# Kernel tuning notes

Hardware: AMD Instinct MI355X
Metric: run time of the kernel (lower is better)

Reference implementation:

```python
import jax, jax.numpy as jnp
import numpy as np

N = 4096
DIM = 128      # dim_in
HID = 256      # mlp hidden_dim
K_IN = 8       # k for linear_k

def _knn_edges(dist, k):
    # dist: [n,n]; k nearest neighbors excluding self (matches heapq loop)
    n = dist.shape[0]
    d = jnp.where(jnp.eye(n, dtype=bool), jnp.inf, dist)
    nbr = jax.lax.top_k(-d, k)[1]                     # [n,k] indices of k smallest
    src = jnp.repeat(jnp.arange(n), k)                # res[0] = i
    dst = nbr.reshape(-1)                             # res[1] = neighbor
    return src, dst

def _gcn_conv(x, src, dst, W, b):
    # torch_geometric GCNConv: add self loops + symmetric normalization
    n = x.shape[0]
    loop = jnp.arange(n)
    s = jnp.concatenate([src, loop])
    t = jnp.concatenate([dst, loop])
    xw = x @ W
    deg = jax.ops.segment_sum(jnp.ones(s.shape[0], x.dtype), t, num_segments=n)
    dinv = jax.lax.rsqrt(deg)                         # deg >= 1 due to self loops
    norm = dinv[s] * dinv[t]
    out = jax.ops.segment_sum(norm[:, None] * xw[s], t, num_segments=n)
    return out + b

def _gcn(x, src, dst, Wg1, bg1, Wg2, bg2):
    h = jax.nn.relu(_gcn_conv(x, src, dst, Wg1, bg1))
    h = _gcn_conv(h, src, dst, Wg2, bg2)              # dropout is identity in eval
    return jax.nn.log_softmax(h, axis=1)

def _conv2d(x, w, b):
    y = jax.lax.conv_general_dilated(x, w, (1, 1), 'SAME',
        dimension_numbers=('NCHW', 'OIHW', 'NCHW'))
    return y + b.reshape(1, -1, 1, 1)

def setup_inputs():
    key = jax.random.key(0)
    ks = jax.random.split(key, 20)
    f32 = jnp.float32
    def w(k, shape):
        fan = shape[0]
        return (jax.random.uniform(k, shape, f32) * 2 - 1) * (1.0 / np.sqrt(fan))
    return {
        'data_x_1': jax.random.normal(ks[0], (1, N, 4), f32),
        'data_x_2': jax.random.normal(ks[1], (1, N, K_IN, 4), f32),
        'Wk': w(ks[2], (K_IN, 1)),        'bk': jnp.zeros((1,), f32),
        'Wg1': w(ks[3], (8, DIM // 2)),   'bg1': jnp.zeros((DIM // 2,), f32),
        'Wg2': w(ks[4], (DIM // 2, DIM)), 'bg2': jnp.zeros((DIM,), f32),
        'Wq': w(ks[5], (3 * DIM, DIM)),   'bq': jnp.zeros((DIM,), f32),
        'Wkey': w(ks[6], (3 * DIM, DIM)), 'bkey': jnp.zeros((DIM,), f32),
        'Woff': w(ks[7], (4, DIM)),       'boff': jnp.zeros((DIM,), f32),
        'pw': jnp.full((1,), 0.25, f32),
        'Wf1': w(ks[8], (DIM, HID)),      'bf1': jnp.zeros((HID,), f32),
        'Wf2': w(ks[9], (HID, HID)),      'bf2': jnp.zeros((HID,), f32),
        'Wf3': w(ks[10], (HID, 4)),       'bf3': jnp.zeros((4,), f32),
        'Wcy3': w(ks[11], (1, 1, 1, 3)),  'bcy3': jnp.zeros((1,), f32),
        'Wcx3': w(ks[12], (1, 1, 3, 1)),  'bcx3': jnp.zeros((1,), f32),
        'Wcy5': w(ks[13], (1, 1, 1, 5)),  'bcy5': jnp.zeros((1,), f32),
        'Wcx5': w(ks[14], (1, 1, 5, 1)),  'bcx5': jnp.zeros((1,), f32),
        'Wcy9': w(ks[15], (1, 1, 1, 9)),  'bcy9': jnp.zeros((1,), f32),
        'Wcx9': w(ks[16], (1, 1, 9, 1)),  'bcx9': jnp.zeros((1,), f32),
    }

def reference(data_x_1, data_x_2, Wk, bk, Wg1, bg1, Wg2, bg2, Wq, bq, Wkey, bkey,
              Woff, boff, pw, Wf1, bf1, Wf2, bf2, Wf3, bf3,
              Wcy3, bcy3, Wcx3, bcx3, Wcy5, bcy5, Wcx5, bcx5, Wcy9, bcy9, Wcx9, bcx9):
    # linear_k over k dimension: [1,n,k,4] -> transpose -> [1,n,4,k] -> [1,n,4]
    dx2 = jnp.swapaxes(data_x_2, 2, 3)
    dx2_out = (dx2 @ Wk + bk)[..., 0]
    data_x = jnp.concatenate([data_x_1, dx2_out], axis=2)   # [1,n,8]
    Ot = data_x[:, :, 4:]                                   # [1,n,4]

    pos = data_x[:, :, 0:2]
    diff = pos[:, :, None, :] - pos[:, None, :, :]          # [1,n,n,2]
    distances = jnp.linalg.norm(diff, axis=3)               # [1,n,n]
    maxd = jnp.max(distances, axis=2, keepdims=True)
    oushi_atte = 1.0 - distances / maxd                     # [1,n,n]

    x0 = data_x[0]
    dist0 = jax.lax.stop_gradient(distances[0])             # knn on detached dist
    embs = []
    for kk in (3, 5, 9):
        src, dst = _knn_edges(dist0, kk)
        embs.append(_gcn(x0, src, dst, Wg1, bg1, Wg2, bg2)[None])
    embedding = jnp.concatenate(embs, axis=2)               # [1,n,3*DIM]

    query = embedding @ Wq + bq                             # [1,n,DIM]
    key_t = embedding @ Wkey + bkey
    scores = jnp.einsum('bnd,bmd->bnm', query, key_t) / jnp.sqrt(jnp.float32(DIM))
    A = scores / jnp.max(scores, axis=2, keepdims=True)     # [1,n,n]

    A4 = A[None]                                            # [1,1,n,n]
    c3 = _conv2d(A4, Wcy3, bcy3) + _conv2d(A4, Wcx3, bcx3)
    c5 = _conv2d(A4, Wcy5, bcy5) + _conv2d(A4, Wcx5, bcx5)
    c9 = _conv2d(A4, Wcy9, bcy9) + _conv2d(A4, Wcx9, bcx9)

    A_cat = jnp.concatenate([A, oushi_atte, c3[0], c5[0], c9[0]], axis=2)  # [1,n,5n]
    A_cat = (A_cat - A_cat.min()) / (A_cat.max() - A_cat.min())

    Ot5 = jnp.tile(Ot, (1, 5, 1))                           # [1,5n,4]
    h = jnp.matmul(A_cat, Ot5)                              # [1,n,4]
    h = h @ Woff + boff                                     # [1,n,DIM]
    h = jnp.where(h > 0, h, pw * h)                         # PReLU (scalar weight)
    h = jax.nn.relu(h @ Wf1 + bf1)
    h = jax.nn.relu(h @ Wf2 + bf2)
    return h @ Wf3 + bf3                                    # [1,n,4]
```

## Files before the change

kernel.cpp:

```cpp
#include <hip/hip_runtime.h>
#include <math.h>

#define NN 4096

static __device__ __forceinline__ unsigned enc_f(float f){
    unsigned u = __float_as_uint(f);
    return (u & 0x80000000u) ? ~u : (u | 0x80000000u);
}
static __device__ __forceinline__ float dec_f(unsigned u){
    unsigned b = (u & 0x80000000u) ? (u & 0x7fffffffu) : ~u;
    return __uint_as_float(b);
}

__global__ void k_prep(const float* __restrict__ dx1, const float* __restrict__ dx2,
                       const float* __restrict__ Wk, const float* __restrict__ bk,
                       float* __restrict__ x0, float* __restrict__ colsum){
    int n = blockIdx.x*blockDim.x + threadIdx.x;
    if (n >= NN) return;
    float wk[8];
    #pragma unroll
    for (int j=0;j<8;j++) wk[j] = Wk[j];
    float bkv = bk[0];
    #pragma unroll
    for (int c=0;c<4;c++) x0[n*8+c] = dx1[n*4+c];
    #pragma unroll
    for (int c=0;c<4;c++){
        float acc = bkv;
        #pragma unroll
        for (int j=0;j<8;j++) acc += dx2[(n*8+j)*4+c]*wk[j];
        x0[n*8+4+c] = acc;
        atomicAdd(&colsum[c], acc);
    }
}

__global__ __launch_bounds__(256) void k_dist(const float* __restrict__ dx1,
        float* __restrict__ maxd, int* __restrict__ nbr,
        int* __restrict__ cnt3, int* __restrict__ cnt5, int* __restrict__ cnt9){
    __shared__ float2 ps[NN];
    int tid = threadIdx.x;
    for (int j=tid; j<NN; j+=256){
        float4 v = *(const float4*)&dx1[j*4];
        ps[j] = make_float2(v.x, v.y);
    }
    __syncthreads();
    int lane = tid & 63;
    int i = blockIdx.x*4 + (tid>>6);
    float2 pi = ps[i];
    unsigned long long best[9];
    #pragma unroll
    for (int q=0;q<9;q++) best[q] = ~0ULL;
    float lmax = 0.f;
    for (int t=0;t<64;t++){
        int j = (t<<6) | lane;
        float2 p = ps[j];
        float dx = pi.x - p.x, dy = pi.y - p.y;
        float d = sqrtf(dx*dx + dy*dy);
        lmax = fmaxf(lmax, d);
        unsigned long long cand = ((unsigned long long)__float_as_uint(d) << 32) | (unsigned)j;
        if (j != i && cand < best[8]){
            best[8] = cand;
            #pragma unroll
            for (int q=8; q>0; --q){
                if (best[q] < best[q-1]){ unsigned long long tm=best[q]; best[q]=best[q-1]; best[q-1]=tm; }
            }
        }
    }
    #pragma unroll
    for (int m=1;m<64;m<<=1) lmax = fmaxf(lmax, __shfl_xor(lmax, m, 64));
    if (lane==0) maxd[i] = lmax;
    for (int t=0;t<9;t++){
        unsigned long long w = best[0];
        #pragma unroll
        for (int m=1;m<64;m<<=1){
            unsigned long long o = __shfl_xor(w, m, 64);
            if (o < w) w = o;
        }
        if (best[0] == w){
            #pragma unroll
            for (int q=0;q<8;q++) best[q] = best[q+1];
            best[8] = ~0ULL;
        }
        if (lane==0){
            int j = (int)(w & 0xffffffffu);
            nbr[i*9+t] = j;
            atomicAdd(&cnt9[j], 1);
            if (t<5) atomicAdd(&cnt5[j], 1);
            if (t<3) atomicAdd(&cnt3[j], 1);
        }
    }
}

__global__ __launch_bounds__(256) void k_scan(const int* __restrict__ cnt3,
        const int* __restrict__ cnt5, const int* __restrict__ cnt9,
        int* __restrict__ offc, float* __restrict__ dinvc){
    __shared__ int part[256];
    int tid = threadIdx.x;
    for (int g=0; g<3; g++){
        const int* cp = g==0?cnt3:(g==1?cnt5:cnt9);
        int base = tid*16;
        int loc[16]; int s=0;
        #pragma unroll
        for (int q=0;q<16;q++){ loc[q]=s; s += cp[base+q]; }
        part[tid]=s; __syncthreads();
        for (int d=1; d<256; d<<=1){
            int v = (tid>=d) ? part[tid-d] : 0;
            __syncthreads();
            part[tid] += v;
            __syncthreads();
        }
        int pre = (tid==0) ? 0 : part[tid-1];
        #pragma unroll
        for (int q=0;q<16;q++){
            offc[g*NN + base + q]  = pre + loc[q];
            dinvc[g*NN + base + q] = rsqrtf((float)cp[base+q] + 1.f);
        }
        __syncthreads();
    }
}

__global__ void k_fill(const int* __restrict__ nbr, const int* __restrict__ offc,
        int* __restrict__ cur, int* __restrict__ rev){
    int i = blockIdx.x*256 + threadIdx.x;
    if (i >= NN) return;
    #pragma unroll
    for (int t=0;t<9;t++){
        int j = nbr[i*9+t];
        int gmin = t<3 ? 0 : (t<5 ? 1 : 2);
        for (int g=gmin; g<3; g++){
            int pos = atomicAdd(&cur[g*NN+j], 1);
            int rb = (g==0) ? 0 : (g==1 ? NN*3 : NN*8);
            rev[rb + offc[g*NN+j] + pos] = i;
        }
    }
}

__global__ void k_y1(const float* __restrict__ x0, const float* __restrict__ Wg1,
                     float* __restrict__ xw){
    int idx = blockIdx.x*256 + threadIdx.x;
    if (idx >= NN*64) return;
    int n = idx>>6, c = idx&63;
    float acc = 0.f;
    #pragma unroll
    for (int k=0;k<8;k++) acc += x0[n*8+k]*Wg1[k*64+c];
    xw[idx] = acc;
}

__global__ __launch_bounds__(256) void k_h1y2(const float* __restrict__ xw,
        const int* __restrict__ offc,
        const int* __restrict__ cnt3, const int* __restrict__ cnt5, const int* __restrict__ cnt9,
        const int* __restrict__ rev, const float* __restrict__ dinvc,
        const float* __restrict__ bg1, const float* __restrict__ Wg2,
        float* __restrict__ y2){
    __shared__ float h1s[12][64];
    int n0 = blockIdx.x*4, tid = threadIdx.x;
    for (int s=tid; s<768; s+=256){
        int p = s>>6, k = s&63, g = p>>2, n = n0+(p&3);
        const int* cp = g==0?cnt3:(g==1?cnt5:cnt9);
        int rb = (g==0) ? 0 : (g==1 ? NN*3 : NN*8);
        int cnt = cp[n];
        int o = rb + offc[g*NN+n];
        float dv = dinvc[g*NN+n];
        float srow = dv*xw[n*64+k];
        for (int e=0;e<cnt;e++){
            int i = rev[o+e];
            srow += dinvc[g*NN+i]*xw[i*64+k];
        }
        float v = dv*srow + bg1[k];
        h1s[p][k] = v>0.f ? v : 0.f;
    }
    __syncthreads();
    int c = tid & 127, ph = tid>>7;
    float a6[6] = {0,0,0,0,0,0};
    for (int k=0;k<64;k++){
        float w = Wg2[k*128+c];
        #pragma unroll
        for (int q=0;q<6;q++) a6[q] += h1s[q*2+ph][k]*w;
    }
    #pragma unroll
    for (int q=0;q<6;q++){
        int p = q*2+ph, g = p>>2, n = n0+(p&3);
        float dv = dinvc[g*NN+n];
        y2[(size_t)g*NN*128 + (size_t)n*128 + c] = dv*a6[q];
    }
}

__global__ __launch_bounds__(128) void k_fin(const float* __restrict__ y2,
        const int* __restrict__ offc,
        const int* __restrict__ cnt3, const int* __restrict__ cnt5, const int* __restrict__ cnt9,
        const int* __restrict__ rev, const float* __restrict__ dinvc,
        const float* __restrict__ bg2, float* __restrict__ emb){
    __shared__ float sm[2], ss[2];
    int b = blockIdx.x;
    int n = b & (NN-1), g = b >> 12;
    const int* cp = g==0?cnt3:(g==1?cnt5:cnt9);
    int rb = (g==0) ? 0 : (g==1 ? NN*3 : NN*8);
    int cnt = cp[n];
    int o = rb + offc[g*NN+n];
    float dv = dinvc[g*NN+n];
    int c = threadIdx.x;
    const float* yg = y2 + (size_t)g*NN*128;
    float s = yg[(size_t)n*128 + c];
    for (int e=0;e<cnt;e++){
        int i = rev[o+e];
        s += yg[(size_t)i*128 + c];
    }
    float v = dv*s + bg2[c];
    float m = v;
    #pragma unroll
    for (int st=1;st<64;st<<=1) m = fmaxf(m, __shfl_xor(m, st, 64));
    if ((c&63)==0) sm[c>>6] = m;
    __syncthreads();
    m = fmaxf(sm[0], sm[1]);
    float e = expf(v - m);
    float t = e;
    #pragma unroll
    for (int st=1;st<64;st<<=1) t += __shfl_xor(t, st, 64);
    if ((c&63)==0) ss[c>>6] = t;
    __syncthreads();
    t = ss[0]+ss[1];
    emb[n*384 + g*128 + c] = v - m - logf(t);
}

__global__ __launch_bounds__(256) void k_qk(const float* __restrict__ emb,
        const float* __restrict__ Wq, const float* __restrict__ bq,
        const float* __restrict__ Wkey, const float* __restrict__ bkey,
        float* __restrict__ q, float* __restrict__ kbuf){
    __shared__ float es[8][384];
    int n0 = blockIdx.x*8;
    int tid = threadIdx.x;
    for (int idx=tid; idx<8*384; idx+=256){
        int m = idx/384, k = idx%384;
        es[m][k] = emb[(n0+m)*384+k];
    }
    __syncthreads();
    int c = tid & 127;
    int sel = tid >> 7;
    const float* W = sel ? Wkey : Wq;
    float b = sel ? bkey[c] : bq[c];
    float acc[8];
    #pragma unroll
    for (int m=0;m<8;m++) acc[m]=b;
    for (int k=0;k<384;k++){
        float w = W[k*128+c];
        #pragma unroll
        for (int m=0;m<8;m++) acc[m] += es[m][k]*w;
    }
    float* out = sel ? kbuf : q;
    #pragma unroll
    for (int m=0;m<8;m++) out[(n0+m)*128+c] = acc[m];
}

__global__ __launch_bounds__(256) void k_scores(const float* __restrict__ q,
        const float* __restrict__ kb, float* __restrict__ scores,
        unsigned* __restrict__ rowmaxenc, unsigned* __restrict__ rowminenc){
    __shared__ float at[32][132];
    __shared__ float bt[32][132];
    int bx = blockIdx.x & 31;
    int by = blockIdx.x >> 5;
    int r0 = by*128, c0 = bx*128;
    int tid = threadIdx.x;
    int tx = tid & 15, ty = tid >> 4;
    float acc[8][8] = {};
    for (int k0 = 0; k0 < 128; k0 += 32){
        __syncthreads();
        #pragma unroll
        for (int l=0; l<4; l++){
            int idx = tid + l*256;
            int rowi = idx >> 3;
            int kq  = (idx & 7) * 4;
            float4 a = *(const float4*)&q [(size_t)(r0+rowi)*128 + k0 + kq];
            float4 b = *(const float4*)&kb[(size_t)(c0+rowi)*128 + k0 + kq];
            at[kq+0][rowi]=a.x; at[kq+1][rowi]=a.y; at[kq+2][rowi]=a.z; at[kq+3][rowi]=a.w;
            bt[kq+0][rowi]=b.x; bt[kq+1][rowi]=b.y; bt[kq+2][rowi]=b.z; bt[kq+3][rowi]=b.w;
        }
        __syncthreads();
        #pragma unroll
        for (int k=0;k<32;k++){
            float4 a0 = *(const float4*)&at[k][ty*4];
            float4 a1 = *(const float4*)&at[k][64+ty*4];
            float4 b0 = *(const float4*)&bt[k][tx*4];
            float4 b1 = *(const float4*)&bt[k][64+tx*4];
            float av[8] = {a0.x,a0.y,a0.z,a0.w,a1.x,a1.y,a1.z,a1.w};
            float bv[8] = {b0.x,b0.y,b0.z,b0.w,b1.x,b1.y,b1.z,b1.w};
            #pragma unroll
            for (int u=0;u<8;u++){
                #pragma unroll
                for (int v=0;v<8;v++) acc[u][v] += av[u]*bv[v];
            }
        }
    }
    #pragma unroll
    for (int u=0;u<8;u++){
        int rr = r0 + ((u<4)? ty*4+u : 64+ty*4+(u-4));
        float4 s0 = {acc[u][0],acc[u][1],acc[u][2],acc[u][3]};
        float4 s1 = {acc[u][4],acc[u][5],acc[u][6],acc[u][7]};
        *(float4*)&scores[(size_t)rr*NN + c0 + tx*4] = s0;
        *(float4*)&scores[(size_t)rr*NN + c0 + 64 + tx*4] = s1;
        float m = acc[u][0], mn = acc[u][0];
        #pragma unroll
        for (int v=1;v<8;v++){ m = fmaxf(m, acc[u][v]); mn = fminf(mn, acc[u][v]); }
        #pragma unroll
        for (int s=1;s<16;s<<=1){
            m  = fmaxf(m,  __shfl_xor(m,  s, 64));
            mn = fminf(mn, __shfl_xor(mn, s, 64));
        }
        if (tx==0){
            atomicMax(&rowmaxenc[rr], enc_f(m));
            atomicMin(&rowminenc[rr], enc_f(mn));
        }
    }
}

__global__ __launch_bounds__(256) void k_mcat(const float* __restrict__ scores,
        const unsigned* __restrict__ rowmaxenc, const float* __restrict__ maxd,
        const float* __restrict__ dx1, const float* __restrict__ x0,
        const float* __restrict__ Wcy3, const float* __restrict__ Wcx3,
        const float* __restrict__ Wcy5, const float* __restrict__ Wcx5,
        const float* __restrict__ Wcy9, const float* __restrict__ Wcx9,
        const float* __restrict__ bcy3, const float* __restrict__ bcx3,
        const float* __restrict__ bcy5, const float* __restrict__ bcx5,
        const float* __restrict__ bcy9, const float* __restrict__ bcx9,
        float* __restrict__ mnmx, float* __restrict__ hpart){
    __shared__ float As[72][96];
    __shared__ float invr_s[72];
    __shared__ float4 ots[64];
    __shared__ float2 pjv[64];
    __shared__ float2 piv[64];
    __shared__ float ims[64];
    __shared__ float smn[4], smx[4];
    int bx = blockIdx.x, by = blockIdx.y;
    int i0 = by*64, j0 = bx*64;
    int tid = threadIdx.x;

    float wy3[3],wx3[3],wy5[5],wx5[5],wy9[9],wx9[9];
    #pragma unroll
    for (int t=0;t<3;t++){ wy3[t]=Wcy3[t]; wx3[t]=Wcx3[t]; }
    #pragma unroll
    for (int t=0;t<5;t++){ wy5[t]=Wcy5[t]; wx5[t]=Wcx5[t]; }
    #pragma unroll
    for (int t=0;t<9;t++){ wy9[t]=Wcy9[t]; wx9[t]=Wcx9[t]; }
    float bc3 = bcy3[0]+bcx3[0];
    float bc5 = bcy5[0]+bcx5[0];
    float bc9 = bcy9[0]+bcx9[0];

    if (tid < 72){
        int gr = i0-4+tid;
        invr_s[tid] = ((unsigned)gr < NN) ? 1.f/dec_f(rowmaxenc[gr]) : 0.f;
    } else if (tid >= 96 && tid < 160){
        int c = tid-96, j = j0+c;
        float4 v = *(const float4*)&dx1[j*4];
        pjv[c] = make_float2(v.x, v.y);
        ots[c] = *(const float4*)&x0[j*8+4];
    } else if (tid >= 160 && tid < 224){
        int r = tid-160;
        float4 v = *(const float4*)&dx1[(i0+r)*4];
        piv[r] = make_float2(v.x, v.y);
        ims[r] = 1.f/maxd[i0+r];
    }
    __syncthreads();

    bool colEdge = (bx == 0) || (bx == 63);
    for (int s = tid; s < 72*20; s += 256){
        int row = s/20, c4 = s - row*20;
        int gr = i0 - 4 + row;
        int grc = gr < 0 ? 0 : (gr > NN-1 ? NN-1 : gr);
        int gcf = j0 - 8 + c4*4;
        float iv = invr_s[row];
        float4 v;
        if (!colEdge){
            v = *(const float4*)&scores[(size_t)grc*NN + gcf];
        } else {
            v = make_float4(0.f,0.f,0.f,0.f);
            const float* rp = &scores[(size_t)grc*NN];
            if ((unsigned)(gcf+0) < NN) v.x = rp[gcf+0];
            if ((unsigned)(gcf+1) < NN) v.y = rp[gcf+1];
            if ((unsigned)(gcf+2) < NN) v.z = rp[gcf+2];
            if ((unsigned)(gcf+3) < NN) v.w = rp[gcf+3];
        }
        int sc4 = c4 ^ ((row & 3) << 1);
        float* dst = &As[row][sc4*4];
        dst[0]=v.x*iv; dst[1]=v.y*iv; dst[2]=v.z*iv; dst[3]=v.w*iv;
    }
    __syncthreads();

    int rp = tid >> 3, cg = tid & 7;
    int r0l = rp*2;
    float mn = INFINITY, mx = -INFINITY;
    float pdx[2]={0,0}, pdy[2]={0,0}, pdz[2]={0,0}, pdw[2]={0,0};
    float2 prow0 = piv[r0l], prow1 = piv[r0l+1];
    float im0 = ims[r0l], im1 = ims[r0l+1];

    for (int h = 0; h < 2; ++h){
        int cbase = cg*8 + h*4;
        float colw[10][4];
        #pragma unroll
        for (int u=0; u<10; ++u){
            int row = r0l+u;
            int c4 = ((cbase+8)>>2) ^ ((row&3)<<1);
            float4 v = *(const float4*)&As[row][c4*4];
            colw[u][0]=v.x; colw[u][1]=v.y; colw[u][2]=v.z; colw[u][3]=v.w;
        }
        #pragma unroll
        for (int d=0; d<2; ++d){
            int row = r0l+4+d;
            float w[12];
            {
                int c4l = ((cbase+4)>>2) ^ ((row&3)<<1);
                int c4r = ((cbase+12)>>2) ^ ((row&3)<<1);
                float4 l = *(const float4*)&As[row][c4l*4];
                float4 rgt = *(const float4*)&As[row][c4r*4];
                w[0]=l.x; w[1]=l.y; w[2]=l.z; w[3]=l.w;
                #pragma unroll
                for (int k=0;k<4;++k) w[4+k] = colw[4+d][k];
                w[8]=rgt.x; w[9]=rgt.y; w[10]=rgt.z; w[11]=rgt.w;
            }
            float2 prow = d ? prow1 : prow0;
            float imv = d ? im1 : im0;
            #pragma unroll
            for (int c=0;c<4;++c){
                float cx9 = 0.f, cx5 = 0.f, cx3 = 0.f;
                #pragma unroll
                for (int u=0;u<9;++u) cx9 += colw[u+d][c]*wx9[u];
                #pragma unroll
                for (int u=0;u<5;++u) cx5 += colw[u+2+d][c]*wx5[u];
                #pragma unroll
                for (int u=0;u<3;++u) cx3 += colw[u+3+d][c]*wx3[u];
                float cy9 = bc9, cy5 = bc5, cy3 = bc3;
                #pragma unroll
                for (int u=0;u<9;++u) cy9 += w[c+u]*wy9[u];
                #pragma unroll
                for (int u=0;u<5;++u) cy5 += w[c+2+u]*wy5[u];
                #pragma unroll
                for (int u=0;u<3;++u) cy3 += w[c+3+u]*wy3[u];
                float c3v = cy3+cx3, c5v = cy5+cx5, c9v = cy9+cx9;
                mn = fminf(mn, fminf(fminf(c3v,c5v),c9v));
                mx = fmaxf(mx, fmaxf(fmaxf(c3v,c5v),c9v));
                float a = colw[4+d][c];
                float2 pj2 = pjv[cbase+c];
                float ddx = prow.x - pj2.x, ddy = prow.y - pj2.y;
                float ou = 1.f - sqrtf(ddx*ddx + ddy*ddy)*imv;
                float Mv = a + ou + c3v + c5v + c9v;
                float4 ot = ots[cbase+c];
                if (d==0){ pdx[0]+=Mv*ot.x; pdy[0]+=Mv*ot.y; pdz[0]+=Mv*ot.z; pdw[0]+=Mv*ot.w; }
                else     { pdx[1]+=Mv*ot.x; pdy[1]+=Mv*ot.y; pdz[1]+=Mv*ot.z; pdw[1]+=Mv*ot.w; }
            }
        }
    }
    #pragma unroll
    for (int m=1; m<8; m<<=1){
        #pragma unroll
        for (int d=0; d<2; ++d){
            pdx[d] += __shfl_xor(pdx[d], m, 64);
            pdy[d] += __shfl_xor(pdy[d], m, 64);
            pdz[d] += __shfl_xor(pdz[d], m, 64);
            pdw[d] += __shfl_xor(pdw[d], m, 64);
        }
    }
    if (cg == 0){
        #pragma unroll
        for (int d=0; d<2; ++d){
            float4 pd = {pdx[d], pdy[d], pdz[d], pdw[d]};
            *(float4*)&hpart[((size_t)(i0 + r0l + d)*64 + bx)*4] = pd;
        }
    }
    #pragma unroll
    for (int m=1; m<64; m<<=1){
        mn = fminf(mn, __shfl_xor(mn, m, 64));
        mx = fmaxf(mx, __shfl_xor(mx, m, 64));
    }
    int wid = tid >> 6;
    if ((tid & 63) == 0){ smn[wid] = mn; smx[wid] = mx; }
    __syncthreads();
    if (tid == 0){
        float a0 = fminf(fminf(smn[0],smn[1]), fminf(smn[2],smn[3]));
        float b0 = fmaxf(fmaxf(smx[0],smx[1]), fmaxf(smx[2],smx[3]));
        int bid = by*64 + bx;
        mnmx[bid] = a0;
        mnmx[4096 + bid] = b0;
    }
}

__global__ __launch_bounds__(256) void k_gmm(const float* __restrict__ mnmx,
        const unsigned* __restrict__ rowminenc, const unsigned* __restrict__ rowmaxenc,
        float* __restrict__ gmm){
    __shared__ float smn[256], smx[256];
    int tid = threadIdx.x;
    float mn = 0.f, mx = 1.f;
    for (int i=tid; i<4096; i+=256){
        mn = fminf(mn, mnmx[i]);
        mx = fmaxf(mx, mnmx[4096+i]);
        float rmx = dec_f(rowmaxenc[i]);
        float q = dec_f(rowminenc[i]) / rmx;
        mn = fminf(mn, fminf(1.f, q));
        mx = fmaxf(mx, fmaxf(1.f, q));
    }
    smn[tid]=mn; smx[tid]=mx; __syncthreads();
    for (int s=128;s>0;s>>=1){
        if (tid<s){ smn[tid]=fminf(smn[tid],smn[tid+s]); smx[tid]=fmaxf(smx[tid],smx[tid+s]); }
        __syncthreads();
    }
    if (tid==0){ gmm[0]=smn[0]; gmm[1]=smx[0]; }
}

__global__ __launch_bounds__(256) void k_hred(const float* __restrict__ hpart,
        const float* __restrict__ gmm, const float* __restrict__ colsum,
        float* __restrict__ hfin){
    int i = blockIdx.x*256 + threadIdx.x;
    if (i >= NN) return;
    float4 sum = {0,0,0,0};
    const float4* hp = (const float4*)hpart + (size_t)i*64;
    for (int xb=0; xb<64; xb++){
        float4 v = hp[xb];
        sum.x+=v.x; sum.y+=v.y; sum.z+=v.z; sum.w+=v.w;
    }
    float mnv = gmm[0], mxv = gmm[1];
    float s = 1.f/(mxv-mnv), o = -mnv*s;
    float4 cs = *(const float4*)colsum;
    float4 out;
    out.x = s*sum.x + 5.f*o*cs.x;
    out.y = s*sum.y + 5.f*o*cs.y;
    out.z = s*sum.z + 5.f*o*cs.z;
    out.w = s*sum.w + 5.f*o*cs.w;
    *(float4*)&hfin[i*4] = out;
}

__global__ __launch_bounds__(256) void k_mlp(const float* __restrict__ hfin,
        const float* __restrict__ Woff, const float* __restrict__ boff, const float* __restrict__ pw,
        const float* __restrict__ Wf1, const float* __restrict__ bf1,
        const float* __restrict__ Wf2, const float* __restrict__ bf2,
        const float* __restrict__ Wf3, const float* __restrict__ bf3,
        float* __restrict__ out){
    __shared__ float h1[8][128];
    __shared__ float h2[8][256];
    __shared__ float h3[8][256];
    __shared__ float4 red4[256];
    int n0 = blockIdx.x*8, tid = threadIdx.x;
    float p = pw[0];
    {
        int c = tid & 127, mb = (tid>>7)*4;
        #pragma unroll
        for (int mm=0; mm<4; mm++){
            int m = mb+mm;
            float v = boff[c];
            #pragma unroll
            for (int k=0;k<4;k++) v += hfin[(n0+m)*4+k]*Woff[k*128+c];
            h1[m][c] = v>0.f ? v : p*v;
        }
    }
    __syncthreads();
    {
        int c = tid;
        float acc[8];
        #pragma unroll
        for (int m=0;m<8;m++) acc[m] = bf1[c];
        for (int k=0;k<128;k++){
            float w = Wf1[k*256+c];
            #pragma unroll
            for (int m=0;m<8;m++) acc[m] += h1[m][k]*w;
        }
        #pragma unroll
        for (int m=0;m<8;m++) h2[m][c] = acc[m]>0.f?acc[m]:0.f;
    }
    __syncthreads();
    {
        int c = tid;
        float acc[8];
        #pragma unroll
        for (int m=0;m<8;m++) acc[m] = bf2[c];
        for (int k=0;k<256;k++){
            float w = Wf2[k*256+c];
            #pragma unroll
            for (int m=0;m<8;m++) acc[m] += h2[m][k]*w;
        }
        #pragma unroll
        for (int m=0;m<8;m++) h3[m][c] = acc[m]>0.f?acc[m]:0.f;
    }
    __syncthreads();
    float w3_0 = Wf3[tid*4+0], w3_1 = Wf3[tid*4+1], w3_2 = Wf3[tid*4+2], w3_3 = Wf3[tid*4+3];
    for (int m=0;m<8;m++){
        float hv = h3[m][tid];
        float4 r; r.x = hv*w3_0; r.y = hv*w3_1; r.z = hv*w3_2; r.w = hv*w3_3;
        red4[tid]=r; __syncthreads();
        for (int s=128;s>0;s>>=1){
            if(tid<s){
                red4[tid].x+=red4[tid+s].x; red4[tid].y+=red4[tid+s].y;
                red4[tid].z+=red4[tid+s].z; red4[tid].w+=red4[tid+s].w;
            }
            __syncthreads();
        }
        if (tid==0){
            float4 o;
            o.x = red4[0].x + bf3[0]; o.y = red4[0].y + bf3[1];
            o.z = red4[0].z + bf3[2]; o.w = red4[0].w + bf3[3];
            *(float4*)&out[(n0+m)*4] = o;
        }
        __syncthreads();
    }
}

extern "C" void kernel_launch(void* const* d_in, const int* in_sizes, int n_in,
                              void* d_out, int out_size, void* d_ws, size_t ws_size,
                              hipStream_t stream){
    const float* dx1  = (const float*)d_in[0];
    const float* dx2  = (const float*)d_in[1];
    const float* Wk   = (const float*)d_in[2];
    const float* bk   = (const float*)d_in[3];
    const float* Wg1  = (const float*)d_in[4];
    const float* bg1  = (const float*)d_in[5];
    const float* Wg2  = (const float*)d_in[6];
    const float* bg2  = (const float*)d_in[7];
    const float* Wq   = (const float*)d_in[8];
    const float* bq   = (const float*)d_in[9];
    const float* Wkey = (const float*)d_in[10];
    const float* bkey = (const float*)d_in[11];
    const float* Woff = (const float*)d_in[12];
    const float* boff = (const float*)d_in[13];
    const float* pw   = (const float*)d_in[14];
    const float* Wf1  = (const float*)d_in[15];
    const float* bf1  = (const float*)d_in[16];
    const float* Wf2  = (const float*)d_in[17];
    const float* bf2  = (const float*)d_in[18];
    const float* Wf3  = (const float*)d_in[19];
    const float* bf3  = (const float*)d_in[20];
    const float* Wcy3 = (const float*)d_in[21];
    const float* bcy3 = (const float*)d_in[22];
    const float* Wcx3 = (const float*)d_in[23];
    const float* bcx3 = (const float*)d_in[24];
    const float* Wcy5 = (const float*)d_in[25];
    const float* bcy5 = (const float*)d_in[26];
    const float* Wcx5 = (const float*)d_in[27];
    const float* bcx5 = (const float*)d_in[28];
    const float* Wcy9 = (const float*)d_in[29];
    const float* bcy9 = (const float*)d_in[30];
    const float* Wcx9 = (const float*)d_in[31];
    const float* bcx9 = (const float*)d_in[32];

    char* ws = (char*)d_ws;
    size_t off = 0;
    auto alloc = [&](size_t b)->void*{ void* p = ws + off; off += (b + 255) & ~(size_t)255; return p; };

    char* zbase = ws + off;
    float*    colsum    = (float*)   alloc(4*4);
    int*      cnt3      = (int*)     alloc((size_t)NN*4);
    int*      cnt5      = (int*)     alloc((size_t)NN*4);
    int*      cnt9      = (int*)     alloc((size_t)NN*4);
    int*      cur       = (int*)     alloc((size_t)3*NN*4);
    unsigned* rowmaxenc = (unsigned*)alloc((size_t)NN*4);
    size_t zbytes = (size_t)((ws + off) - zbase);
    unsigned* rowminenc = (unsigned*)alloc((size_t)NN*4);

    float* x0     = (float*)alloc((size_t)NN*8*4);
    float* maxd   = (float*)alloc((size_t)NN*4);
    int*   nbr    = (int*)  alloc((size_t)NN*9*4);
    int*   offc   = (int*)  alloc((size_t)3*NN*4);
    float* dinvc  = (float*)alloc((size_t)3*NN*4);
    int*   rev    = (int*)  alloc((size_t)NN*17*4);
    float* xw     = (float*)alloc((size_t)NN*64*4);
    float* y2     = (float*)alloc((size_t)3*NN*128*4);
    float* emb    = (float*)alloc((size_t)NN*384*4);
    float* qb     = (float*)alloc((size_t)NN*128*4);
    float* kb     = (float*)alloc((size_t)NN*128*4);
    float* scores = (float*)alloc((size_t)NN*NN*4);
    float* mnmx   = (float*)alloc((size_t)2*4096*4);
    float* hpart  = (float*)alloc((size_t)NN*64*4*4);
    float* gmm    = (float*)alloc(2*4);
    float* hfin   = (float*)alloc((size_t)NN*4*4);
    (void)ws_size; (void)in_sizes; (void)n_in; (void)out_size;

    hipMemsetAsync(zbase, 0, zbytes, stream);
    hipMemsetAsync(rowminenc, 0xFF, (size_t)NN*4, stream);

    k_prep<<<16,256,0,stream>>>(dx1,dx2,Wk,bk,x0,colsum);
    k_dist<<<NN/4,256,0,stream>>>(dx1,maxd,nbr,cnt3,cnt5,cnt9);
    k_scan<<<1,256,0,stream>>>(cnt3,cnt5,cnt9,offc,dinvc);
    k_fill<<<16,256,0,stream>>>(nbr,offc,cur,rev);

    k_y1  <<<NN*64/256,256,0,stream>>>(x0,Wg1,xw);
    k_h1y2<<<NN/4,256,0,stream>>>(xw,offc,cnt3,cnt5,cnt9,rev,dinvc,bg1,Wg2,y2);
    k_fin <<<NN*3,128,0,stream>>>(y2,offc,cnt3,cnt5,cnt9,rev,dinvc,bg2,emb);

    k_qk<<<NN/8,256,0,stream>>>(emb,Wq,bq,Wkey,bkey,qb,kb);
    k_scores<<<1024,256,0,stream>>>(qb,kb,scores,rowmaxenc,rowminenc);
    k_mcat<<<dim3(64,64),256,0,stream>>>(scores,rowmaxenc,maxd,dx1,x0,
        Wcy3,Wcx3,Wcy5,Wcx5,Wcy9,Wcx9,
        bcy3,bcx3,bcy5,bcx5,bcy9,bcx9, mnmx, hpart);
    k_gmm<<<1,256,0,stream>>>(mnmx,rowminenc,rowmaxenc,gmm);
    k_hred<<<NN/256,256,0,stream>>>(hpart,gmm,colsum,hfin);
    k_mlp<<<NN/8,256,0,stream>>>(hfin,Woff,boff,pw,Wf1,bf1,Wf2,bf2,Wf3,bf3,(float*)d_out);
}
```

Measured before the change: 335.0 us.

## Split conv/matmul fusion into streaming min/max pass and algebraic row-dot reduction

Reformulates the A_cat @ Ot5 product algebraically. Because the convolutions are linear, their contribution to h is computed as row dot-products of the scaled scores against Ot and against a precomputed vertically-convolved Ot (Ty), plus a horizontal 9-tap combination of those per-row results. The distance term is folded into the k_dist kernel as dOt. The convolution values themselves are still needed for the global min/max, so a new streaming kernel computes them per column with a rolling 9-row register window and wave-level LDS exchange, but no longer does the matmul. This removes the big hpart partial buffer and its reduction, at the cost of reading the scores matrix twice (k_cstream and k_rowdot) and changing floating-point summation order.

```diff
diff --git a/kernel.cpp b/kernel.cpp
--- a/kernel.cpp
+++ b/kernel.cpp
@@ -33,9 +33,37 @@
     }
 }
 
+__global__ void k_ty(const float* __restrict__ x0,
+        const float* __restrict__ Wcy3, const float* __restrict__ Wcy5, const float* __restrict__ Wcy9,
+        float* __restrict__ Ty){
+    int j = blockIdx.x*256 + threadIdx.x;
+    if (j >= NN) return;
+    float Cy[9];
+    #pragma unroll
+    for (int o=-4;o<=4;o++){
+        float c = Wcy9[o+4];
+        if (o>=-2 && o<=2) c += Wcy5[o+2];
+        if (o>=-1 && o<=1) c += Wcy3[o+1];
+        Cy[o+4] = c;
+    }
+    float4 acc = {0,0,0,0};
+    #pragma unroll
+    for (int o=-4;o<=4;o++){
+        int jj = j - o;
+        if ((unsigned)jj < NN){
+            float4 ot = *(const float4*)&x0[jj*8+4];
+            float c = Cy[o+4];
+            acc.x += c*ot.x; acc.y += c*ot.y; acc.z += c*ot.z; acc.w += c*ot.w;
+        }
+    }
+    *(float4*)&Ty[j*4] = acc;
+}
+
 __global__ __launch_bounds__(256) void k_dist(const float* __restrict__ dx1,
+        const float* __restrict__ x0,
         float* __restrict__ maxd, int* __restrict__ nbr,
-        int* __restrict__ cnt3, int* __restrict__ cnt5, int* __restrict__ cnt9){
+        int* __restrict__ cnt3, int* __restrict__ cnt5, int* __restrict__ cnt9,
+        float* __restrict__ dOt){
     __shared__ float2 ps[NN];
     int tid = threadIdx.x;
     for (int j=tid; j<NN; j+=256){
@@ -50,12 +78,15 @@
     #pragma unroll
     for (int q=0;q<9;q++) best[q] = ~0ULL;
     float lmax = 0.f;
+    float4 dacc = {0,0,0,0};
     for (int t=0;t<64;t++){
         int j = (t<<6) | lane;
         float2 p = ps[j];
         float dx = pi.x - p.x, dy = pi.y - p.y;
         float d = sqrtf(dx*dx + dy*dy);
         lmax = fmaxf(lmax, d);
+        float4 otj = *(const float4*)&x0[j*8+4];
+        dacc.x += d*otj.x; dacc.y += d*otj.y; dacc.z += d*otj.z; dacc.w += d*otj.w;
         unsigned long long cand = ((unsigned long long)__float_as_uint(d) << 32) | (unsigned)j;
         if (j != i && cand < best[8]){
             best[8] = cand;
@@ -66,8 +97,17 @@
         }
     }
     #pragma unroll
-    for (int m=1;m<64;m<<=1) lmax = fmaxf(lmax, __shfl_xor(lmax, m, 64));
-    if (lane==0) maxd[i] = lmax;
+    for (int m=1;m<64;m<<=1){
+        lmax = fmaxf(lmax, __shfl_xor(lmax, m, 64));
+        dacc.x += __shfl_xor(dacc.x, m, 64);
+        dacc.y += __shfl_xor(dacc.y, m, 64);
+        dacc.z += __shfl_xor(dacc.z, m, 64);
+        dacc.w += __shfl_xor(dacc.w, m, 64);
+    }
+    if (lane==0){
+        maxd[i] = lmax;
+        *(float4*)&dOt[i*4] = dacc;
+    }
     for (int t=0;t<9;t++){
         unsigned long long w = best[0];
         #pragma unroll
@@ -311,26 +351,31 @@
     }
 }
 
-__global__ __launch_bounds__(256) void k_mcat(const float* __restrict__ scores,
-        const unsigned* __restrict__ rowmaxenc, const float* __restrict__ maxd,
-        const float* __restrict__ dx1, const float* __restrict__ x0,
+__global__ void k_invr(const unsigned* __restrict__ rowmaxenc, const float* __restrict__ maxd,
+        float* __restrict__ invr, float* __restrict__ im){
+    int i = blockIdx.x*256 + threadIdx.x;
+    if (i >= NN) return;
+    invr[i] = 1.f/dec_f(rowmaxenc[i]);
+    im[i]   = 1.f/maxd[i];
+}
+
+__global__ __launch_bounds__(256) void k_cstream(const float* __restrict__ scores,
+        const float* __restrict__ invr,
         const float* __restrict__ Wcy3, const float* __restrict__ Wcx3,
         const float* __restrict__ Wcy5, const float* __restrict__ Wcx5,
         const float* __restrict__ Wcy9, const float* __restrict__ Wcx9,
         const float* __restrict__ bcy3, const float* __restrict__ bcx3,
         const float* __restrict__ bcy5, const float* __restrict__ bcx5,
         const float* __restrict__ bcy9, const float* __restrict__ bcx9,
-        float* __restrict__ mnmx, float* __restrict__ hpart){
-    __shared__ float As[72][96];
-    __shared__ float invr_s[72];
-    __shared__ float4 ots[64];
-    __shared__ float2 pjv[64];
-    __shared__ float2 piv[64];
-    __shared__ float ims[64];
+        float* __restrict__ mnmx){
+    __shared__ float rowbuf[4][80];
     __shared__ float smn[4], smx[4];
-    int bx = blockIdx.x, by = blockIdx.y;
-    int i0 = by*64, j0 = bx*64;
     int tid = threadIdx.x;
+    int w = tid >> 6, lane = tid & 63;
+    int jb = blockIdx.x*256 + w*64;
+    int j  = jb + lane;
+    int i0 = blockIdx.y*64;
+    volatile float* rb = rowbuf[w];
 
     float wy3[3],wx3[3],wy5[5],wx5[5],wy9[9],wx9[9];
     #pragma unroll
@@ -343,124 +388,60 @@
     float bc5 = bcy5[0]+bcx5[0];
     float bc9 = bcy9[0]+bcx9[0];
 
-    if (tid < 72){
-        int gr = i0-4+tid;
-        invr_s[tid] = ((unsigned)gr < NN) ? 1.f/dec_f(rowmaxenc[gr]) : 0.f;
-    } else if (tid >= 96 && tid < 160){
-        int c = tid-96, j = j0+c;
-        float4 v = *(const float4*)&dx1[j*4];
-        pjv[c] = make_float2(v.x, v.y);
-        ots[c] = *(const float4*)&x0[j*8+4];
-    } else if (tid >= 160 && tid < 224){
-        int r = tid-160;
-        float4 v = *(const float4*)&dx1[(i0+r)*4];
-        piv[r] = make_float2(v.x, v.y);
-        ims[r] = 1.f/maxd[i0+r];
-    }
-    __syncthreads();
-
-    bool colEdge = (bx == 0) || (bx == 63);
-    for (int s = tid; s < 72*20; s += 256){
-        int row = s/20, c4 = s - row*20;
-        int gr = i0 - 4 + row;
-        int grc = gr < 0 ? 0 : (gr > NN-1 ? NN-1 : gr);
-        int gcf = j0 - 8 + c4*4;
-        float iv = invr_s[row];
-        float4 v;
-        if (!colEdge){
-            v = *(const float4*)&scores[(size_t)grc*NN + gcf];
-        } else {
-            v = make_float4(0.f,0.f,0.f,0.f);
-            const float* rp = &scores[(size_t)grc*NN];
-            if ((unsigned)(gcf+0) < NN) v.x = rp[gcf+0];
-            if ((unsigned)(gcf+1) < NN) v.y = rp[gcf+1];
-            if ((unsigned)(gcf+2) < NN) v.z = rp[gcf+2];
-            if ((unsigned)(gcf+3) < NN) v.w = rp[gcf+3];
-        }
-        int sc4 = c4 ^ ((row & 3) << 1);
-        float* dst = &As[row][sc4*4];
-        dst[0]=v.x*iv; dst[1]=v.y*iv; dst[2]=v.z*iv; dst[3]=v.w*iv;
-    }
-    __syncthreads();
-
-    int rp = tid >> 3, cg = tid & 7;
-    int r0l = rp*2;
+    float win[9], cy3r[9], cy5r[9], cy9r[9];
     float mn = INFINITY, mx = -INFINITY;
-    float pdx[2]={0,0}, pdy[2]={0,0}, pdz[2]={0,0}, pdw[2]={0,0};
-    float2 prow0 = piv[r0l], prow1 = piv[r0l+1];
-    float im0 = ims[r0l], im1 = ims[r0l+1];
-
-    for (int h = 0; h < 2; ++h){
-        int cbase = cg*8 + h*4;
-        float colw[10][4];
-        #pragma unroll
-        for (int u=0; u<10; ++u){
-            int row = r0l+u;
-            int c4 = ((cbase+8)>>2) ^ ((row&3)<<1);
-            float4 v = *(const float4*)&As[row][c4*4];
-            colw[u][0]=v.x; colw[u][1]=v.y; colw[u][2]=v.z; colw[u][3]=v.w;
-        }
-        #pragma unroll
-        for (int d=0; d<2; ++d){
-            int row = r0l+4+d;
-            float w[12];
-            {
-                int c4l = ((cbase+4)>>2) ^ ((row&3)<<1);
-                int c4r = ((cbase+12)>>2) ^ ((row&3)<<1);
-                float4 l = *(const float4*)&As[row][c4l*4];
-                float4 rgt = *(const float4*)&As[row][c4r*4];
-                w[0]=l.x; w[1]=l.y; w[2]=l.z; w[3]=l.w;
-                #pragma unroll
-                for (int k=0;k<4;++k) w[4+k] = colw[4+d][k];
-                w[8]=rgt.x; w[9]=rgt.y; w[10]=rgt.z; w[11]=rgt.w;
+
+    bool haloL = (lane < 4);
+    bool haloR = (lane >= 60);
+    int jL = jb - 4 + lane;
+    int jR = jb + lane + 4;
+    bool vlL = haloL && (jL >= 0);
+    bool vlR = haloR && (jR < NN);
+
+    for (int tb = 0; tb < 8; ++tb){
+        #pragma unroll
+        for (int u = 0; u < 9; ++u){
+            int t  = tb*9 + u;
+            int ri = i0 - 4 + t;
+            bool rv = ((unsigned)ri < NN);
+            float iv = 0.f, v = 0.f, vL = 0.f, vR = 0.f;
+            if (rv){
+                iv = invr[ri];
+                const float* rp = scores + (size_t)ri*NN;
+                v = rp[j];
+                if (vlL) vL = rp[jL];
+                if (vlR) vR = rp[jR];
             }
-            float2 prow = d ? prow1 : prow0;
-            float imv = d ? im1 : im0;
+            float a = v*iv;
+            rb[lane+4] = a;
+            if (haloL) rb[lane]   = vL*iv;
+            if (haloR) rb[lane+8] = vR*iv;
+            __builtin_amdgcn_wave_barrier();
+            float tp[9];
             #pragma unroll
-            for (int c=0;c<4;++c){
-                float cx9 = 0.f, cx5 = 0.f, cx3 = 0.f;
-                #pragma unroll
-                for (int u=0;u<9;++u) cx9 += colw[u+d][c]*wx9[u];
-                #pragma unroll
-                for (int u=0;u<5;++u) cx5 += colw[u+2+d][c]*wx5[u];
-                #pragma unroll
-                for (int u=0;u<3;++u) cx3 += colw[u+3+d][c]*wx3[u];
-                float cy9 = bc9, cy5 = bc5, cy3 = bc3;
-                #pragma unroll
-                for (int u=0;u<9;++u) cy9 += w[c+u]*wy9[u];
-                #pragma unroll
-                for (int u=0;u<5;++u) cy5 += w[c+2+u]*wy5[u];
-                #pragma unroll
-                for (int u=0;u<3;++u) cy3 += w[c+3+u]*wy3[u];
-                float c3v = cy3+cx3, c5v = cy5+cx5, c9v = cy9+cx9;
-                mn = fminf(mn, fminf(fminf(c3v,c5v),c9v));
-                mx = fmaxf(mx, fmaxf(fmaxf(c3v,c5v),c9v));
-                float a = colw[4+d][c];
-                float2 pj2 = pjv[cbase+c];
-                float ddx = prow.x - pj2.x, ddy = prow.y - pj2.y;
-                float ou = 1.f - sqrtf(ddx*ddx + ddy*ddy)*imv;
-                float Mv = a + ou + c3v + c5v + c9v;
-                float4 ot = ots[cbase+c];
-                if (d==0){ pdx[0]+=Mv*ot.x; pdy[0]+=Mv*ot.y; pdz[0]+=Mv*ot.z; pdw[0]+=Mv*ot.w; }
-                else     { pdx[1]+=Mv*ot.x; pdy[1]+=Mv*ot.y; pdz[1]+=Mv*ot.z; pdw[1]+=Mv*ot.w; }
+            for (int k=0;k<9;k++) tp[k] = rb[lane+k];
+            __builtin_amdgcn_wave_barrier();
+            float cy9v = ((tp[0]*wy9[0] + tp[1]*wy9[1]) + (tp[2]*wy9[2] + tp[3]*wy9[3]))
+                       + ((tp[4]*wy9[4] + tp[5]*wy9[5]) + (tp[6]*wy9[6] + tp[7]*wy9[7]))
+                       + tp[8]*wy9[8];
+            float cy5v = ((tp[2]*wy5[0] + tp[3]*wy5[1]) + (tp[4]*wy5[2] + tp[5]*wy5[3]))
+                       + tp[6]*wy5[4];
+            float cy3v = (tp[3]*wy3[0] + tp[4]*wy3[1]) + tp[5]*wy3[2];
+            win[u]  = a;
+            cy3r[u] = cy3v; cy5r[u] = cy5v; cy9r[u] = cy9v;
+            if (t >= 8){
+                float cx9v = ((win[(u+1)%9]*wx9[0] + win[(u+2)%9]*wx9[1]) + (win[(u+3)%9]*wx9[2] + win[(u+4)%9]*wx9[3]))
+                           + ((win[(u+5)%9]*wx9[4] + win[(u+6)%9]*wx9[5]) + (win[(u+7)%9]*wx9[6] + win[(u+8)%9]*wx9[7]))
+                           + win[u]*wx9[8];
+                float cx5v = ((win[(u+3)%9]*wx5[0] + win[(u+4)%9]*wx5[1]) + (win[(u+5)%9]*wx5[2] + win[(u+6)%9]*wx5[3]))
+                           + win[(u+7)%9]*wx5[4];
+                float cx3v = (win[(u+4)%9]*wx3[0] + win[(u+5)%9]*wx3[1]) + win[(u+6)%9]*wx3[2];
+                float c9 = cy9r[(u+5)%9] + cx9v + bc9;
+                float c5 = cy5r[(u+5)%9] + cx5v + bc5;
+                float c3 = cy3r[(u+5)%9] + cx3v + bc3;
+                mn = fminf(mn, fminf(fminf(c3,c5),c9));
+                mx = fmaxf(mx, fmaxf(fmaxf(c3,c5),c9));
             }
-        }
-    }
-    #pragma unroll
-    for (int m=1; m<8; m<<=1){
-        #pragma unroll
-        for (int d=0; d<2; ++d){
-            pdx[d] += __shfl_xor(pdx[d], m, 64);
-            pdy[d] += __shfl_xor(pdy[d], m, 64);
-            pdz[d] += __shfl_xor(pdz[d], m, 64);
-            pdw[d] += __shfl_xor(pdw[d], m, 64);
-        }
-    }
-    if (cg == 0){
-        #pragma unroll
-        for (int d=0; d<2; ++d){
-            float4 pd = {pdx[d], pdy[d], pdz[d], pdw[d]};
-            *(float4*)&hpart[((size_t)(i0 + r0l + d)*64 + bx)*4] = pd;
         }
     }
     #pragma unroll
@@ -468,15 +449,59 @@
         mn = fminf(mn, __shfl_xor(mn, m, 64));
         mx = fmaxf(mx, __shfl_xor(mx, m, 64));
     }
-    int wid = tid >> 6;
-    if ((tid & 63) == 0){ smn[wid] = mn; smx[wid] = mx; }
+    if (lane == 0){ smn[w] = mn; smx[w] = mx; }
     __syncthreads();
     if (tid == 0){
         float a0 = fminf(fminf(smn[0],smn[1]), fminf(smn[2],smn[3]));
         float b0 = fmaxf(fmaxf(smx[0],smx[1]), fmaxf(smx[2],smx[3]));
-        int bid = by*64 + bx;
+        int bid = blockIdx.y*16 + blockIdx.x;
         mnmx[bid] = a0;
-        mnmx[4096 + bid] = b0;
+        mnmx[1024 + bid] = b0;
+    }
+}
+
+__global__ __launch_bounds__(256) void k_rowdot(const float* __restrict__ scores,
+        const float* __restrict__ x0, const float* __restrict__ Ty,
+        const float* __restrict__ invr, const float* __restrict__ im,
+        const float* __restrict__ dOt, const float* __restrict__ colsum,
+        const float* __restrict__ bcy3, const float* __restrict__ bcx3,
+        const float* __restrict__ bcy5, const float* __restrict__ bcx5,
+        const float* __restrict__ bcy9, const float* __restrict__ bcx9,
+        float* __restrict__ ASdot, float* __restrict__ Bv){
+    int tid = threadIdx.x;
+    int tc = tid & 31, tr = tid >> 5;
+    int i = blockIdx.x*8 + tr;
+    const float* srow = scores + (size_t)i*NN;
+    float4 ss = {0,0,0,0}, st = {0,0,0,0};
+    for (int c0 = tc; c0 < NN; c0 += 32){
+        float sv = srow[c0];
+        float4 ot = *(const float4*)&x0[c0*8+4];
+        float4 ty = *(const float4*)&Ty[c0*4];
+        ss.x += sv*ot.x; ss.y += sv*ot.y; ss.z += sv*ot.z; ss.w += sv*ot.w;
+        st.x += sv*ty.x; st.y += sv*ty.y; st.z += sv*ty.z; st.w += sv*ty.w;
+    }
+    #pragma unroll
+    for (int s=1; s<32; s<<=1){
+        ss.x += __shfl_xor(ss.x, s, 64); ss.y += __shfl_xor(ss.y, s, 64);
+        ss.z += __shfl_xor(ss.z, s, 64); ss.w += __shfl_xor(ss.w, s, 64);
+        st.x += __shfl_xor(st.x, s, 64); st.y += __shfl_xor(st.y, s, 64);
+        st.z += __shfl_xor(st.z, s, 64); st.w += __shfl_xor(st.w, s, 64);
+    }
+    if (tc == 0){
+        float iv = invr[i], imv = im[i];
+        float bcsum = bcy3[0]+bcx3[0]+bcy5[0]+bcx5[0]+bcy9[0]+bcx9[0];
+        float4 cs = *(const float4*)colsum;
+        float4 dv = *(const float4*)&dOt[i*4];
+        float4 as;
+        as.x = iv*ss.x; as.y = iv*ss.y; as.z = iv*ss.z; as.w = iv*ss.w;
+        float k = 1.f + bcsum;
+        float4 b;
+        b.x = cs.x*k - imv*dv.x + iv*st.x;
+        b.y = cs.y*k - imv*dv.y + iv*st.y;
+        b.z = cs.z*k - imv*dv.z + iv*st.z;
+        b.w = cs.w*k - imv*dv.w + iv*st.w;
+        *(float4*)&ASdot[i*4] = as;
+        *(float4*)&Bv[i*4]   = b;
     }
 }
 
@@ -486,14 +511,16 @@
     __shared__ float smn[256], smx[256];
     int tid = threadIdx.x;
     float mn = 0.f, mx = 1.f;
-    for (int i=tid; i<4096; i+=256){
-        mn = fminf(mn, mnmx[i]);
-        mx = fmaxf(mx, mnmx[4096+i]);
+    for (int i=tid; i<NN; i+=256){
         float rmx = dec_f(rowmaxenc[i]);
         float q = dec_f(rowminenc[i]) / rmx;
         mn = fminf(mn, fminf(1.f, q));
         mx = fmaxf(mx, fmaxf(1.f, q));
     }
+    for (int b=tid; b<1024; b+=256){
+        mn = fminf(mn, mnmx[b]);
+        mx = fmaxf(mx, mnmx[1024+b]);
+    }
     smn[tid]=mn; smx[tid]=mx; __syncthreads();
     for (int s=128;s>0;s>>=1){
         if (tid<s){ smn[tid]=fminf(smn[tid],smn[tid+s]); smx[tid]=fmaxf(smx[tid],smx[tid+s]); }
@@ -502,25 +529,40 @@
     if (tid==0){ gmm[0]=smn[0]; gmm[1]=smx[0]; }
 }
 
-__global__ __launch_bounds__(256) void k_hred(const float* __restrict__ hpart,
+__global__ void k_hfin(const float* __restrict__ ASdot, const float* __restrict__ Bv,
+        const float* __restrict__ Wcx3, const float* __restrict__ Wcx5, const float* __restrict__ Wcx9,
         const float* __restrict__ gmm, const float* __restrict__ colsum,
         float* __restrict__ hfin){
     int i = blockIdx.x*256 + threadIdx.x;
     if (i >= NN) return;
-    float4 sum = {0,0,0,0};
-    const float4* hp = (const float4*)hpart + (size_t)i*64;
-    for (int xb=0; xb<64; xb++){
-        float4 v = hp[xb];
-        sum.x+=v.x; sum.y+=v.y; sum.z+=v.z; sum.w+=v.w;
+    float Cx[9];
+    #pragma unroll
+    for (int o=-4;o<=4;o++){
+        float c = Wcx9[o+4];
+        if (o>=-2 && o<=2) c += Wcx5[o+2];
+        if (o>=-1 && o<=1) c += Wcx3[o+1];
+        Cx[o+4] = c;
+    }
+    float4 h = *(const float4*)&Bv[i*4];
+    float4 a0 = *(const float4*)&ASdot[i*4];
+    h.x += a0.x; h.y += a0.y; h.z += a0.z; h.w += a0.w;
+    #pragma unroll
+    for (int o=-4;o<=4;o++){
+        int r = i + o;
+        if ((unsigned)r < NN){
+            float4 av = *(const float4*)&ASdot[r*4];
+            float c = Cx[o+4];
+            h.x += c*av.x; h.y += c*av.y; h.z += c*av.z; h.w += c*av.w;
+        }
     }
     float mnv = gmm[0], mxv = gmm[1];
-    float s = 1.f/(mxv-mnv), o = -mnv*s;
+    float s = 1.f/(mxv-mnv), oa = -mnv*s;
     float4 cs = *(const float4*)colsum;
     float4 out;
-    out.x = s*sum.x + 5.f*o*cs.x;
-    out.y = s*sum.y + 5.f*o*cs.y;
-    out.z = s*sum.z + 5.f*o*cs.z;
-    out.w = s*sum.w + 5.f*o*cs.w;
+    out.x = s*h.x + 5.f*oa*cs.x;
+    out.y = s*h.y + 5.f*oa*cs.y;
+    out.z = s*h.z + 5.f*oa*cs.z;
+    out.w = s*h.w + 5.f*oa*cs.w;
     *(float4*)&hfin[i*4] = out;
 }
 
@@ -661,8 +703,13 @@
     float* qb     = (float*)alloc((size_t)NN*128*4);
     float* kb     = (float*)alloc((size_t)NN*128*4);
     float* scores = (float*)alloc((size_t)NN*NN*4);
-    float* mnmx   = (float*)alloc((size_t)2*4096*4);
-    float* hpart  = (float*)alloc((size_t)NN*64*4*4);
+    float* Tyb    = (float*)alloc((size_t)NN*4*4);
+    float* invr   = (float*)alloc((size_t)NN*4);
+    float* im     = (float*)alloc((size_t)NN*4);
+    float* dOt    = (float*)alloc((size_t)NN*4*4);
+    float* ASd    = (float*)alloc((size_t)NN*4*4);
+    float* Bv     = (float*)alloc((size_t)NN*4*4);
+    float* mnmx   = (float*)alloc((size_t)2*1024*4);
     float* gmm    = (float*)alloc(2*4);
     float* hfin   = (float*)alloc((size_t)NN*4*4);
     (void)ws_size; (void)in_sizes; (void)n_in; (void)out_size;
@@ -671,7 +718,8 @@
     hipMemsetAsync(rowminenc, 0xFF, (size_t)NN*4, stream);
 
     k_prep<<<16,256,0,stream>>>(dx1,dx2,Wk,bk,x0,colsum);
-    k_dist<<<NN/4,256,0,stream>>>(dx1,maxd,nbr,cnt3,cnt5,cnt9);
+    k_ty  <<<16,256,0,stream>>>(x0,Wcy3,Wcy5,Wcy9,Tyb);
+    k_dist<<<NN/4,256,0,stream>>>(dx1,x0,maxd,nbr,cnt3,cnt5,cnt9,dOt);
     k_scan<<<1,256,0,stream>>>(cnt3,cnt5,cnt9,offc,dinvc);
     k_fill<<<16,256,0,stream>>>(nbr,offc,cur,rev);
 
@@ -681,10 +729,14 @@
 
     k_qk<<<NN/8,256,0,stream>>>(emb,Wq,bq,Wkey,bkey,qb,kb);
     k_scores<<<1024,256,0,stream>>>(qb,kb,scores,rowmaxenc,rowminenc);
-    k_mcat<<<dim3(64,64),256,0,stream>>>(scores,rowmaxenc,maxd,dx1,x0,
+    k_invr<<<16,256,0,stream>>>(rowmaxenc,maxd,invr,im);
+
+    k_cstream<<<dim3(16,64),256,0,stream>>>(scores,invr,
         Wcy3,Wcx3,Wcy5,Wcx5,Wcy9,Wcx9,
-        bcy3,bcx3,bcy5,bcx5,bcy9,bcx9, mnmx, hpart);
+        bcy3,bcx3,bcy5,bcx5,bcy9,bcx9, mnmx);
+    k_rowdot<<<NN/8,256,0,stream>>>(scores,x0,Tyb,invr,im,dOt,colsum,
+        bcy3,bcx3,bcy5,bcx5,bcy9,bcx9, ASd, Bv);
     k_gmm<<<1,256,0,stream>>>(mnmx,rowminenc,rowmaxenc,gmm);
-    k_hred<<<NN/256,256,0,stream>>>(hpart,gmm,colsum,hfin);
+    k_hfin<<<16,256,0,stream>>>(ASd,Bv,Wcx3,Wcx5,Wcx9,gmm,colsum,hfin);
     k_mlp<<<NN/8,256,0,stream>>>(hfin,Woff,boff,pw,Wf1,bf1,Wf2,bf2,Wf3,bf3,(float*)d_out);
 }
```

Result: slower. 407.2 us (+21.6%).
